# Performance work log

Hardware: AMD Instinct MI355X
Metric: run time of the kernel (lower is better)

Reference implementation:

```python
import jax, jax.numpy as jnp
import numpy as np

DIM = 1024
HEADS = 16
HIDDEN = 4096
EPS_ATTN = 1e-6
EPS_LN = 1e-5


def layer_norm(x, g, b):
    mu = jnp.mean(x, axis=-1, keepdims=True)
    var = jnp.var(x, axis=-1, keepdims=True)
    return (x - mu) * jax.lax.rsqrt(var + EPS_LN) * g + b


def setup_inputs() -> dict:
    key = jax.random.key(0)
    ks = jax.random.split(key, 8)
    s = 0.02
    return {
        "x": jax.random.normal(ks[0], (4, 4096, DIM), jnp.float32),
        "norm1_g": jnp.ones((DIM,), jnp.float32),
        "norm1_b": jnp.zeros((DIM,), jnp.float32),
        "qkv_w": jax.random.normal(ks[1], (3 * DIM, DIM), jnp.float32) * s,  # torch Linear layout [out,in]
        "proj_w": jax.random.normal(ks[2], (DIM, DIM), jnp.float32) * s,
        "proj_b": jnp.zeros((DIM,), jnp.float32),
        "norm2_g": jnp.ones((DIM,), jnp.float32),
        "norm2_b": jnp.zeros((DIM,), jnp.float32),
        "fc1_w": jax.random.normal(ks[3], (HIDDEN, DIM), jnp.float32) * s,
        "fc1_b": jnp.zeros((HIDDEN,), jnp.float32),
        "fc2_w": jax.random.normal(ks[4], (DIM, HIDDEN), jnp.float32) * s,
        "fc2_b": jnp.zeros((DIM,), jnp.float32),
    }


def reference(x, norm1_g, norm1_b, qkv_w, proj_w, proj_b, norm2_g, norm2_b,
              fc1_w, fc1_b, fc2_w, fc2_b):
    B, N, C = x.shape
    H = HEADS
    d = C // H

    # ---- linear attention on norm1(x) ----
    h = layer_norm(x, norm1_g, norm1_b)
    qkv = jnp.einsum("bnc,oc->bno", h, qkv_w)           # [B,N,3C]
    qkv = qkv.reshape(B, N, 3, H, d)
    q = jnp.transpose(qkv[:, :, 0], (0, 2, 1, 3))        # [B,H,N,d]
    k = jnp.transpose(qkv[:, :, 1], (0, 2, 1, 3))
    v = jnp.transpose(qkv[:, :, 2], (0, 2, 1, 3))

    q = jax.nn.elu(q) + 1.0                              # phi(Q)
    k = jax.nn.elu(k) + 1.0                              # phi(K)

    kv = jnp.einsum("bhnd,bhne->bhde", k, v)             # [B,H,d,d]
    ksum = jnp.sum(k, axis=2)                            # [B,H,d]
    z = 1.0 / (jnp.einsum("bhnd,bhd->bhn", q, ksum) + EPS_ATTN)  # [B,H,N]
    attn_out = jnp.einsum("bhnd,bhde->bhne", q, kv) * z[..., None]
    attn_out = jnp.transpose(attn_out, (0, 2, 1, 3)).reshape(B, N, C)
    attn_out = jnp.einsum("bnc,oc->bno", attn_out, proj_w) + proj_b

    x = x + attn_out

    # ---- MLP on norm2(x) ----
    h = layer_norm(x, norm2_g, norm2_b)
    h = jax.nn.gelu(jnp.einsum("bnc,hc->bnh", h, fc1_w) + fc1_b, approximate=False)
    h = jnp.einsum("bnh,ch->bnc", h, fc2_w) + fc2_b
    return x + h
```

## Files before the change

kernel.cpp:

```cpp
#include <hip/hip_runtime.h>
#include <stdint.h>
#include <math.h>


#define TOK   16384
#define CDIM  1024
#define NHEAD 16
#define HD    64
#define SEQ   4096
#define NBH   64
#define HID   4096

typedef unsigned short u16;
typedef __attribute__((ext_vector_type(8))) short bf16x8;
typedef __attribute__((ext_vector_type(4))) float f32x4;
typedef __attribute__((ext_vector_type(4))) unsigned short u16x4;

__device__ __forceinline__ u16 f2bf(float f) {
  union { float f; uint32_t u; } c; c.f = f;
  uint32_t u = c.u;
  return (u16)((u + 0x7fffu + ((u >> 16) & 1u)) >> 16);
}
__device__ __forceinline__ float bf2f(u16 h) {
  union { uint32_t u; float f; } c; c.u = ((uint32_t)h) << 16;
  return c.f;
}
__device__ __forceinline__ float gelu_fast(float u) {
  float y = 1.5957691216f * (u + 0.044715f * u * u * u);
  return u * __builtin_amdgcn_rcpf(1.0f + __expf(-y));
}

typedef const __attribute__((address_space(1))) uint32_t* gas_t;
typedef __attribute__((address_space(3))) uint32_t* las_t;
__device__ __forceinline__ void gl_lds16(const u16* g, u16* l) {
  __builtin_amdgcn_global_load_lds((gas_t)g, (las_t)l, 16, 0, 0);
}

__global__ __launch_bounds__(256) void cvt_kernel(const float* __restrict__ in,
                                                  u16* __restrict__ out, int n4) {
  int i = blockIdx.x * 256 + threadIdx.x;
  if (i < n4) {
    float4 v = ((const float4*)in)[i];
    u16x4 o;
    o.x = f2bf(v.x); o.y = f2bf(v.y); o.z = f2bf(v.z); o.w = f2bf(v.w);
    ((u16x4*)out)[i] = o;
  }
}

__global__ __launch_bounds__(256) void ln_kernel(const float* __restrict__ xin,
                                                 const float* __restrict__ g,
                                                 const float* __restrict__ b,
                                                 u16* __restrict__ out) {
  int row = blockIdx.x;
  int t = threadIdx.x;
  const float4* xr = (const float4*)(xin + (size_t)row * CDIM);
  float4 v = xr[t];
  float s  = v.x + v.y + v.z + v.w;
  float s2 = v.x * v.x + v.y * v.y + v.z * v.z + v.w * v.w;
#pragma unroll
  for (int off = 32; off > 0; off >>= 1) {
    s  += __shfl_down(s, off);
    s2 += __shfl_down(s2, off);
  }
  __shared__ float as_[4], bs_[4];
  if ((t & 63) == 0) { as_[t >> 6] = s; bs_[t >> 6] = s2; }
  __syncthreads();
  s  = as_[0] + as_[1] + as_[2] + as_[3];
  s2 = bs_[0] + bs_[1] + bs_[2] + bs_[3];
  float mu  = s * (1.0f / CDIM);
  float var = s2 * (1.0f / CDIM) - mu * mu;
  float rs  = rsqrtf(var + 1e-5f);
  float4 gv = ((const float4*)g)[t];
  float4 bv = ((const float4*)b)[t];
  u16x4 o;
  o.x = f2bf((v.x - mu) * rs * gv.x + bv.x);
  o.y = f2bf((v.y - mu) * rs * gv.y + bv.y);
  o.z = f2bf((v.z - mu) * rs * gv.z + bv.z);
  o.w = f2bf((v.w - mu) * rs * gv.w + bv.w);
  ((u16x4*)(out + (size_t)row * CDIM))[t] = o;
}

enum { M_QKV = 0, M_PROJ = 1, M_FC1 = 2, M_FC2 = 3 };

#define BARRIER() do { asm volatile("" ::: "memory"); \
                       __builtin_amdgcn_s_barrier();  \
                       asm volatile("" ::: "memory"); } while (0)
#define WAITV(n)  asm volatile("s_waitcnt vmcnt(" #n ")" ::: "memory")

#define LDA(c, mh) do { \
  _Pragma("unroll") for (int mf = 0; mf < 4; ++mf) \
  _Pragma("unroll") for (int s = 0; s < 2; ++s) \
    a_[mf][s] = *(const bf16x8*)(ldsb + (c) * 65536 + abyte[mh][mf] + s * 64); \
} while (0)

#define LDB(c, nh, dst) do { \
  _Pragma("unroll") for (int nf = 0; nf < 2; ++nf) \
  _Pragma("unroll") for (int s = 0; s < 2; ++s) \
    dst[nf][s] = *(const bf16x8*)(ldsb + (c) * 65536 + 32768 + bbyte[nh][nf] + s * 64); \
} while (0)

#define STAGE_A(c, u, kt) do { \
  _Pragma("unroll") for (int i = 0; i < 2; ++i) \
    gl_lds16(Ab + aoff[i] + ((u) ? K64r : 0) + (size_t)(kt) * 64, \
             (u16*)(ldsb + (c) * 65536 + (u) * 16384 + pb[i])); \
} while (0)

#define STAGE_B(c, u, kt) do { \
  _Pragma("unroll") for (int i = 0; i < 2; ++i) \
    gl_lds16(Wb + boff[i] + ((u) ? K32r : 0) + (size_t)(kt) * 64, \
             (u16*)(ldsb + (c) * 65536 + 32768 + (u) * 16384 + pb[i])); \
} while (0)

#define MFMA16(mo, no, B) do { \
  __builtin_amdgcn_s_setprio(1); \
  _Pragma("unroll") for (int s = 0; s < 2; ++s) \
  _Pragma("unroll") for (int mf = 0; mf < 4; ++mf) \
  _Pragma("unroll") for (int nf = 0; nf < 2; ++nf) \
    acc[(mo) + mf][(no) + nf] = __builtin_amdgcn_mfma_f32_16x16x32_bf16( \
        a_[mf][s], B[nf][s], acc[(mo) + mf][(no) + nf], 0, 0, 0); \
  __builtin_amdgcn_s_setprio(0); \
} while (0)

template <int MODE>
__global__ __launch_bounds__(512, 2) void gemm256(const u16* __restrict__ A,
                                                  const u16* __restrict__ W, int K,
                                                  void* __restrict__ o0,
                                                  void* __restrict__ o1,
                                                  void* __restrict__ o2,
                                                  const float* __restrict__ bias,
                                                  const float* __restrict__ resid) {
  __shared__ __align__(16) u16 lds_[65536];
  char* ldsb = (char*)lds_;
  const int t = threadIdx.x;
  const int l = t & 63, w = t >> 6;
  const int wm = w >> 2, wn = w & 3;
  const int fr = l & 15, qq = l >> 4;

  const int nwg = gridDim.x;
  const int wg  = blockIdx.x;
  const int swz = (wg & 7) * (nwg >> 3) + (wg >> 3);
  const int mt = swz & 63, nt = swz >> 6;
  const int m0 = mt * 256, n0 = nt * 256;

  const u16* Ab = A + (size_t)m0 * K;
  const u16* Wb = W + (size_t)n0 * K;
  const size_t K64r = (size_t)K * 64;
  const size_t K32r = (size_t)K * 32;

  size_t aoff[2], boff[2];
  int pb[2];
#pragma unroll
  for (int i = 0; i < 2; ++i) {
    int p = (i * 512 + t) * 16;
    int q = p ^ (((p >> 9) & 1) << 5);
    int prow = q >> 7;
    int kc = (q & 127) >> 1;
    pb[i] = p;
    aoff[i] = (size_t)(((prow >> 6) & 1) * 128 + (prow & 63)) * K + kc;
    boff[i] = (size_t)(((prow >> 5) & 3) * 64 + (prow & 31)) * K + kc;
  }
  int abyte[2][4], bbyte[2][2];
#pragma unroll
  for (int mh = 0; mh < 2; ++mh)
#pragma unroll
    for (int mf = 0; mf < 4; ++mf) {
      int R = wm * 128 + (mh * 4 + mf) * 16 + fr;
      int slot = ((R >> 6) & 1) * 128 + ((R >> 7) & 1) * 64 + (R & 63);
      int qx = qq ^ (((slot >> 2) & 1) << 1);
      abyte[mh][mf] = slot * 128 + qx * 16;
    }
#pragma unroll
  for (int nh = 0; nh < 2; ++nh)
#pragma unroll
    for (int nf = 0; nf < 2; ++nf) {
      int R = wn * 64 + (nh * 2 + nf) * 16 + fr;
      int slot = ((R >> 5) & 1) * 128 + ((R >> 6) & 3) * 32 + (R & 31);
      int qx = qq ^ (((slot >> 2) & 1) << 1);
      bbyte[nh][nf] = slot * 128 + qx * 16;
    }

  f32x4 acc[8][4] = {};
  bf16x8 a_[4][2], b0_[2][2], b1_[2][2];

  const int nkt = K >> 6;
  const int niter = nkt >> 1;

  STAGE_A(0, 0, 0); STAGE_B(0, 0, 0); STAGE_B(0, 1, 0); STAGE_A(0, 1, 0);
  STAGE_A(1, 0, 1); STAGE_B(1, 0, 1); STAGE_B(1, 1, 1);
  WAITV(6);
  BARRIER();

  for (int it = 0; it < niter - 1; ++it) {
    const int t0 = 2 * it;
    LDA(0, 0); LDB(0, 0, b0_);
    STAGE_A(1, 1, t0 + 1);
    BARRIER(); MFMA16(0, 0, b0_); BARRIER();
    LDB(0, 1, b1_);
    STAGE_A(0, 0, t0 + 2);
    BARRIER(); MFMA16(0, 2, b1_); BARRIER();
    LDA(0, 1);
    STAGE_B(0, 0, t0 + 2);
    BARRIER(); MFMA16(4, 2, b1_); BARRIER();
    STAGE_B(0, 1, t0 + 2);
    WAITV(6);
    BARRIER(); MFMA16(4, 0, b0_); BARRIER();
    LDA(1, 0); LDB(1, 0, b0_);
    STAGE_A(0, 1, t0 + 2);
    BARRIER(); MFMA16(0, 0, b0_); BARRIER();
    LDB(1, 1, b1_);
    STAGE_A(1, 0, t0 + 3);
    BARRIER(); MFMA16(0, 2, b1_); BARRIER();
    LDA(1, 1);
    STAGE_B(1, 0, t0 + 3);
    BARRIER(); MFMA16(4, 2, b1_); BARRIER();
    STAGE_B(1, 1, t0 + 3);
    WAITV(6);
    BARRIER(); MFMA16(4, 0, b0_); BARRIER();
  }
  {
    LDA(0, 0); LDB(0, 0, b0_);
    STAGE_A(1, 1, nkt - 1);
    BARRIER(); MFMA16(0, 0, b0_); BARRIER();
    LDB(0, 1, b1_);
    BARRIER(); MFMA16(0, 2, b1_); BARRIER();
    LDA(0, 1);
    BARRIER(); MFMA16(4, 2, b1_); BARRIER();
    WAITV(0);
    BARRIER(); MFMA16(4, 0, b0_); BARRIER();
    LDA(1, 0); LDB(1, 0, b0_);
    BARRIER(); MFMA16(0, 0, b0_); BARRIER();
    LDB(1, 1, b1_);
    BARRIER(); MFMA16(0, 2, b1_); BARRIER();
    LDA(1, 1);
    BARRIER(); MFMA16(4, 2, b1_); BARRIER();
    MFMA16(4, 0, b0_);
  }

#pragma unroll
  for (int mi = 0; mi < 8; ++mi) {
#pragma unroll
    for (int nj = 0; nj < 4; ++nj) {
      int go = n0 + wn * 64 + nj * 16 + fr;
#pragma unroll
      for (int r = 0; r < 4; ++r) {
        int gm = m0 + wm * 128 + mi * 16 + qq * 4 + r;
        float v = acc[mi][nj][r];
        if constexpr (MODE == M_QKV) {
          int sect = go >> 10, c = go & 1023;
          int h = c >> 6, dd = c & 63;
          int b = gm >> 12, n = gm & 4095;
          int bh = b * NHEAD + h;
          if (sect == 0) {
            float qv = v > 0.f ? v + 1.f : __expf(v);
            ((u16*)o0)[((size_t)bh * SEQ + n) * HD + dd] = f2bf(qv);
          } else if (sect == 1) {
            float kk = v > 0.f ? v + 1.f : __expf(v);
            ((u16*)o1)[((size_t)bh * HD + dd) * SEQ + n] = f2bf(kk);
          } else {
            ((u16*)o2)[((size_t)bh * HD + dd) * SEQ + n] = f2bf(v);
          }
        } else if constexpr (MODE == M_PROJ) {
          ((float*)o0)[(size_t)gm * CDIM + go] = v + bias[go] + resid[(size_t)gm * CDIM + go];
        } else if constexpr (MODE == M_FC1) {
          float u = v + bias[go];
          ((u16*)o0)[(size_t)gm * HID + go] = f2bf(gelu_fast(u));
        } else {
          ((float*)o0)[(size_t)gm * CDIM + go] = v + bias[go] + resid[(size_t)gm * CDIM + go];
        }
      }
    }
  }
}

__global__ __launch_bounds__(256) void kv_stage1(const u16* __restrict__ kt,
                                                 const u16* __restrict__ vt,
                                                 float* __restrict__ pkv,
                                                 float* __restrict__ pks) {
  int ch = blockIdx.x, bh = blockIdx.y;
  int t = threadIdx.x, l = t & 63, w = t >> 6;
  int fr = l & 15, qq = l >> 4;
  int nb = ch * 512;
  const u16* vb = vt + (size_t)bh * HD * SEQ;
  const u16* kb = kt + (size_t)bh * HD * SEQ;
  int e0 = (w >> 1) * 32, d0 = (w & 1) * 32;
  f32x4 acc[2][2] = {};
  for (int kk = 0; kk < 512; kk += 32) {
    bf16x8 af[2], bfv[2];
#pragma unroll
    for (int i = 0; i < 2; ++i)
      af[i] = *(const bf16x8*)(vb + (size_t)(e0 + i * 16 + fr) * SEQ + nb + kk + qq * 8);
#pragma unroll
    for (int j = 0; j < 2; ++j)
      bfv[j] = *(const bf16x8*)(kb + (size_t)(d0 + j * 16 + fr) * SEQ + nb + kk + qq * 8);
#pragma unroll
    for (int i = 0; i < 2; ++i)
#pragma unroll
      for (int j = 0; j < 2; ++j)
        acc[i][j] = __builtin_amdgcn_mfma_f32_16x16x32_bf16(af[i], bfv[j], acc[i][j], 0, 0, 0);
  }
  float* pout = pkv + ((size_t)ch * NBH + bh) * 4096;
#pragma unroll
  for (int i = 0; i < 2; ++i)
#pragma unroll
    for (int j = 0; j < 2; ++j)
#pragma unroll
      for (int r = 0; r < 4; ++r) {
        int e = e0 + i * 16 + qq * 4 + r;
        int d = d0 + j * 16 + fr;
        pout[e * 64 + d] = acc[i][j][r];
      }
  __shared__ float ksp[256];
  {
    int d = t & 63, part = t >> 6;
    const u16* kr = kb + (size_t)d * SEQ + nb + part * 128;
    float s = 0;
    for (int n = 0; n < 128; ++n) s += bf2f(kr[n]);
    ksp[t] = s;
  }
  __syncthreads();
  if (t < 64) {
    float s = ksp[t] + ksp[64 + t] + ksp[128 + t] + ksp[192 + t];
    pks[((size_t)ch * NBH + bh) * 64 + t] = s;
  }
}

__global__ __launch_bounds__(256) void kv_reduce(const float* __restrict__ pkv,
                                                 const float* __restrict__ pks,
                                                 u16* __restrict__ kvt,
                                                 float* __restrict__ ksm) {
  int bh = blockIdx.x, t = threadIdx.x;
  for (int ii = 0; ii < 16; ++ii) {
    int idx = ii * 256 + t;
    float s = 0;
#pragma unroll
    for (int c = 0; c < 8; ++c) s += pkv[((size_t)c * NBH + bh) * 4096 + idx];
    kvt[(size_t)bh * 4096 + idx] = f2bf(s);
  }
  if (t < 64) {
    float s = 0;
#pragma unroll
    for (int c = 0; c < 8; ++c) s += pks[((size_t)c * NBH + bh) * 64 + t];
    ksm[bh * 64 + t] = s;
  }
}

__global__ __launch_bounds__(256) void attn_kernel(const u16* __restrict__ qb,
                                                   const u16* __restrict__ kvt,
                                                   const float* __restrict__ ksm,
                                                   u16* __restrict__ ab) {
  int nblk = blockIdx.x, bh = blockIdx.y;
  int n0 = nblk * 128;
  int t = threadIdx.x, l = t & 63, w = t >> 6;
  int fr = l & 15, qq = l >> 4;
  __shared__ float ksh[64];
  __shared__ float part[256];
  __shared__ float zsh[128];
  if (t < 64) ksh[t] = ksm[bh * 64 + t];
  __syncthreads();
  {
    int rr = t >> 1, hf = t & 1;
    const u16* qr = qb + ((size_t)bh * SEQ + n0 + rr) * HD + hf * 32;
    float s = 0;
#pragma unroll
    for (int d = 0; d < 32; ++d) s += bf2f(qr[d]) * ksh[hf * 32 + d];
    part[t] = s;
  }
  __syncthreads();
  if (t < 128) zsh[t] = 1.0f / (part[2 * t] + part[2 * t + 1] + 1e-6f);
  __syncthreads();

  f32x4 acc[2][4] = {};
  const u16* qbase = qb + ((size_t)bh * SEQ + n0) * HD;
  const u16* kvb = kvt + (size_t)bh * 4096;
#pragma unroll
  for (int ks = 0; ks < 64; ks += 32) {
    bf16x8 af[2], bfv[4];
#pragma unroll
    for (int i = 0; i < 2; ++i)
      af[i] = *(const bf16x8*)(qbase + (size_t)(w * 32 + i * 16 + fr) * HD + ks + qq * 8);
#pragma unroll
    for (int j = 0; j < 4; ++j)
      bfv[j] = *(const bf16x8*)(kvb + (size_t)(j * 16 + fr) * HD + ks + qq * 8);
#pragma unroll
    for (int i = 0; i < 2; ++i)
#pragma unroll
      for (int j = 0; j < 4; ++j)
        acc[i][j] = __builtin_amdgcn_mfma_f32_16x16x32_bf16(af[i], bfv[j], acc[i][j], 0, 0, 0);
  }
  int b = bh >> 4, h = bh & 15;
#pragma unroll
  for (int i = 0; i < 2; ++i)
#pragma unroll
    for (int j = 0; j < 4; ++j)
#pragma unroll
      for (int r = 0; r < 4; ++r) {
        int rl = w * 32 + i * 16 + qq * 4 + r;
        int n = n0 + rl;
        int e = j * 16 + fr;
        float v = acc[i][j][r] * zsh[rl];
        ab[((size_t)(b * SEQ + n)) * CDIM + h * HD + e] = f2bf(v);
      }
}

extern "C" void kernel_launch(void* const* d_in, const int* in_sizes, int n_in,
                              void* d_out, int out_size, void* d_ws, size_t ws_size,
                              hipStream_t stream) {
  (void)in_sizes; (void)n_in; (void)out_size; (void)ws_size;
  const float* x     = (const float*)d_in[0];
  const float* n1g   = (const float*)d_in[1];
  const float* n1b   = (const float*)d_in[2];
  const float* qkvw  = (const float*)d_in[3];
  const float* projw = (const float*)d_in[4];
  const float* projb = (const float*)d_in[5];
  const float* n2g   = (const float*)d_in[6];
  const float* n2b   = (const float*)d_in[7];
  const float* fc1w  = (const float*)d_in[8];
  const float* fc1b  = (const float*)d_in[9];
  const float* fc2w  = (const float*)d_in[10];
  const float* fc2b  = (const float*)d_in[11];
  float* out = (float*)d_out;

  char* ws = (char*)d_ws;
  size_t off = 0;
  auto alloc = [&](size_t bytes) {
    void* p = ws + off;
    off += (bytes + 255) & ~(size_t)255;
    return p;
  };
  u16*  wq   = (u16*)alloc((size_t)3 * CDIM * CDIM * 2);
  u16*  wp   = (u16*)alloc((size_t)CDIM * CDIM * 2);
  u16*  w1   = (u16*)alloc((size_t)HID * CDIM * 2);
  u16*  w2   = (u16*)alloc((size_t)CDIM * HID * 2);
  u16*  kvt  = (u16*)alloc((size_t)NBH * 4096 * 2);
  float* ksm = (float*)alloc((size_t)NBH * 64 * 4);
  float* x2  = (float*)alloc((size_t)TOK * CDIM * 4);
  u16*  h12  = (u16*)alloc((size_t)TOK * CDIM * 2);
  u16*  qbuf = (u16*)alloc((size_t)TOK * CDIM * 2);
  u16*  ktb  = (u16*)alloc((size_t)TOK * CDIM * 2);
  u16*  vtb  = (u16*)alloc((size_t)TOK * CDIM * 2);
  u16*  abuf = (u16*)alloc((size_t)TOK * CDIM * 2);
  float* pkv = (float*)abuf;
  float* pks = (float*)(abuf + (size_t)8 * NBH * 4096 * 2);
  u16*  h3   = qbuf;

  cvt_kernel<<<dim3(3 * CDIM * CDIM / 1024), 256, 0, stream>>>(qkvw, wq, 3 * CDIM * CDIM / 4);
  cvt_kernel<<<dim3(CDIM * CDIM / 1024),     256, 0, stream>>>(projw, wp, CDIM * CDIM / 4);
  cvt_kernel<<<dim3(HID * CDIM / 1024),      256, 0, stream>>>(fc1w, w1, HID * CDIM / 4);
  cvt_kernel<<<dim3(CDIM * HID / 1024),      256, 0, stream>>>(fc2w, w2, CDIM * HID / 4);

  ln_kernel<<<dim3(TOK), 256, 0, stream>>>(x, n1g, n1b, h12);
  gemm256<M_QKV><<<dim3(64 * 12), 512, 0, stream>>>(
      h12, wq, CDIM, qbuf, ktb, vtb, nullptr, nullptr);
  kv_stage1<<<dim3(8, NBH), 256, 0, stream>>>(ktb, vtb, pkv, pks);
  kv_reduce<<<dim3(NBH), 256, 0, stream>>>(pkv, pks, kvt, ksm);
  attn_kernel<<<dim3(SEQ / 128, NBH), 256, 0, stream>>>(qbuf, kvt, ksm, abuf);
  gemm256<M_PROJ><<<dim3(64 * 4), 512, 0, stream>>>(
      abuf, wp, CDIM, x2, nullptr, nullptr, projb, x);
  ln_kernel<<<dim3(TOK), 256, 0, stream>>>(x2, n2g, n2b, h12);
  gemm256<M_FC1><<<dim3(64 * 16), 512, 0, stream>>>(
      h12, w1, CDIM, h3, nullptr, nullptr, fc1b, nullptr);
  gemm256<M_FC2><<<dim3(64 * 4), 512, 0, stream>>>(
      h3, w2, HID, out, nullptr, nullptr, fc2b, x2);
}
```

Measured before the change: 792.2 us.

## Rework LDS swizzle, XCD-aware tile mapping, and vectorize QKV epilogue stores

```diff
diff --git a/kernel.cpp b/kernel.cpp
--- a/kernel.cpp
+++ b/kernel.cpp
@@ -90,13 +90,13 @@
 #define LDA(c, mh) do { \
   _Pragma("unroll") for (int mf = 0; mf < 4; ++mf) \
   _Pragma("unroll") for (int s = 0; s < 2; ++s) \
-    a_[mf][s] = *(const bf16x8*)(ldsb + (c) * 65536 + abyte[mh][mf] + s * 64); \
+    a_[mf][s] = *(const bf16x8*)(ldsb + (c) * 65536 + (abyte[mh][mf] ^ (s * 64))); \
 } while (0)
 
 #define LDB(c, nh, dst) do { \
   _Pragma("unroll") for (int nf = 0; nf < 2; ++nf) \
   _Pragma("unroll") for (int s = 0; s < 2; ++s) \
-    dst[nf][s] = *(const bf16x8*)(ldsb + (c) * 65536 + 32768 + bbyte[nh][nf] + s * 64); \
+    dst[nf][s] = *(const bf16x8*)(ldsb + (c) * 65536 + 32768 + (bbyte[nh][nf] ^ (s * 64))); \
 } while (0)
 
 #define STAGE_A(c, u, kt) do { \
@@ -136,10 +136,10 @@
   const int wm = w >> 2, wn = w & 3;
   const int fr = l & 15, qq = l >> 4;
 
-  const int nwg = gridDim.x;
-  const int wg  = blockIdx.x;
-  const int swz = (wg & 7) * (nwg >> 3) + (wg >> 3);
-  const int mt = swz & 63, nt = swz >> 6;
+  const int wg = blockIdx.x;
+  const int xcd = wg & 7, k_ = wg >> 3;
+  const int mt = xcd * 8 + (k_ & 7);
+  const int nt = k_ >> 3;
   const int m0 = mt * 256, n0 = nt * 256;
 
   const u16* Ab = A + (size_t)m0 * K;
@@ -152,8 +152,8 @@
 #pragma unroll
   for (int i = 0; i < 2; ++i) {
     int p = (i * 512 + t) * 16;
-    int q = p ^ (((p >> 9) & 1) << 5);
-    int prow = q >> 7;
+    int q = p ^ (((p >> 7) & 7) << 4);
+    int prow = p >> 7;
     int kc = (q & 127) >> 1;
     pb[i] = p;
     aoff[i] = (size_t)(((prow >> 6) & 1) * 128 + (prow & 63)) * K + kc;
@@ -166,8 +166,7 @@
     for (int mf = 0; mf < 4; ++mf) {
       int R = wm * 128 + (mh * 4 + mf) * 16 + fr;
       int slot = ((R >> 6) & 1) * 128 + ((R >> 7) & 1) * 64 + (R & 63);
-      int qx = qq ^ (((slot >> 2) & 1) << 1);
-      abyte[mh][mf] = slot * 128 + qx * 16;
+      abyte[mh][mf] = slot * 128 + ((qq ^ (slot & 3)) << 4) + (((slot >> 2) & 1) << 6);
     }
 #pragma unroll
   for (int nh = 0; nh < 2; ++nh)
@@ -175,8 +174,7 @@
     for (int nf = 0; nf < 2; ++nf) {
       int R = wn * 64 + (nh * 2 + nf) * 16 + fr;
       int slot = ((R >> 5) & 1) * 128 + ((R >> 6) & 3) * 32 + (R & 31);
-      int qx = qq ^ (((slot >> 2) & 1) << 1);
-      bbyte[nh][nf] = slot * 128 + qx * 16;
+      bbyte[nh][nf] = slot * 128 + ((qq ^ (slot & 3)) << 4) + (((slot >> 2) & 1) << 6);
     }
 
   f32x4 acc[8][4] = {};
@@ -241,31 +239,43 @@
 #pragma unroll
     for (int nj = 0; nj < 4; ++nj) {
       int go = n0 + wn * 64 + nj * 16 + fr;
-#pragma unroll
-      for (int r = 0; r < 4; ++r) {
-        int gm = m0 + wm * 128 + mi * 16 + qq * 4 + r;
-        float v = acc[mi][nj][r];
-        if constexpr (MODE == M_QKV) {
-          int sect = go >> 10, c = go & 1023;
-          int h = c >> 6, dd = c & 63;
-          int b = gm >> 12, n = gm & 4095;
-          int bh = b * NHEAD + h;
-          if (sect == 0) {
+      int gmb = m0 + wm * 128 + mi * 16 + qq * 4;
+      if constexpr (MODE == M_QKV) {
+        int sect = go >> 10, c = go & 1023;
+        int h = c >> 6, dd = c & 63;
+        int b = gmb >> 12, n = gmb & 4095;
+        int bh = b * NHEAD + h;
+        if (sect == 0) {
+#pragma unroll
+          for (int r = 0; r < 4; ++r) {
+            float v = acc[mi][nj][r];
             float qv = v > 0.f ? v + 1.f : __expf(v);
-            ((u16*)o0)[((size_t)bh * SEQ + n) * HD + dd] = f2bf(qv);
-          } else if (sect == 1) {
-            float kk = v > 0.f ? v + 1.f : __expf(v);
-            ((u16*)o1)[((size_t)bh * HD + dd) * SEQ + n] = f2bf(kk);
+            ((u16*)o0)[((size_t)bh * SEQ + n + r) * HD + dd] = f2bf(qv);
+          }
+        } else {
+          u16x4 pk;
+#pragma unroll
+          for (int r = 0; r < 4; ++r) {
+            float v = acc[mi][nj][r];
+            float e = (sect == 1) ? (v > 0.f ? v + 1.f : __expf(v)) : v;
+            pk[r] = f2bf(e);
+          }
+          u16* dst = (sect == 1) ? (u16*)o1 : (u16*)o2;
+          *(u16x4*)(dst + ((size_t)bh * HD + dd) * SEQ + n) = pk;
+        }
+      } else {
+#pragma unroll
+        for (int r = 0; r < 4; ++r) {
+          int gm = gmb + r;
+          float v = acc[mi][nj][r];
+          if constexpr (MODE == M_PROJ) {
+            ((float*)o0)[(size_t)gm * CDIM + go] = v + bias[go] + resid[(size_t)gm * CDIM + go];
+          } else if constexpr (MODE == M_FC1) {
+            float u = v + bias[go];
+            ((u16*)o0)[(size_t)gm * HID + go] = f2bf(gelu_fast(u));
           } else {
-            ((u16*)o2)[((size_t)bh * HD + dd) * SEQ + n] = f2bf(v);
+            ((float*)o0)[(size_t)gm * CDIM + go] = v + bias[go] + resid[(size_t)gm * CDIM + go];
           }
-        } else if constexpr (MODE == M_PROJ) {
-          ((float*)o0)[(size_t)gm * CDIM + go] = v + bias[go] + resid[(size_t)gm * CDIM + go];
-        } else if constexpr (MODE == M_FC1) {
-          float u = v + bias[go];
-          ((u16*)o0)[(size_t)gm * HID + go] = f2bf(gelu_fast(u));
-        } else {
-          ((float*)o0)[(size_t)gm * CDIM + go] = v + bias[go] + resid[(size_t)gm * CDIM + go];
         }
       }
     }
```

Measured after the change: 684.9 us. 1.16x faster.
